# Kernel tuning notes

Measured on AMD Instinct MI355X. Metric: run time of the kernel, lower is better.

## Reference

```python
import jax, jax.numpy as jnp
import numpy as np

# Constants from __init__ (heston_info = [rho, theta, kappa, lambd], asset_info = [S0, V0, rate])
S0 = 100.0
V0 = 0.04
RATE = 0.025
THETA = 0.04
KAPPA = 1.5
LAMBD = 0.3
V_FLOOR = 0.01  # torch: V_old_abs = max(cat([V_new, zeros+0.01]), dim=1)

N_DIM = 3       # MLP input = [time, S, V]
N_LAYERS = 2
WIDTH = 50
MC = 65536
N_STEPS = 252
N_STRIKES = 13
N_MAT = 12


def setup_inputs() -> dict:
    key = jax.random.key(0)
    k = jax.random.split(key, 8)
    z = jax.random.normal(k[0], (MC, N_STEPS), dtype=jnp.float32)
    z1 = jax.random.normal(k[1], (MC, N_STEPS), dtype=jnp.float32)
    strikes_call = jnp.linspace(70.0, 100.0, N_STRIKES).astype(jnp.float32)
    strikes_put = jnp.linspace(100.0, 130.0, N_STRIKES).astype(jnp.float32)
    indices = jnp.arange(1, N_MAT + 1, dtype=jnp.int32) * (N_STEPS // N_MAT)  # monthly maturities
    timegrid = jnp.linspace(0.0, 1.0, N_STEPS + 1, dtype=jnp.float32)
    # 4 stacked MLPs: [drift, diffusion, driftV, diffusionV]; small init keeps the SDE stable
    s = 0.05
    W_in = s * jax.random.normal(k[2], (4, N_DIM, WIDTH), dtype=jnp.float32)
    b_in = jnp.zeros((4, WIDTH), jnp.float32)
    W_h = s * jax.random.normal(k[3], (4, N_LAYERS - 1, WIDTH, WIDTH), dtype=jnp.float32)
    b_h = jnp.zeros((4, N_LAYERS - 1, WIDTH), jnp.float32)
    W_out = 0.01 * jax.random.normal(k[4], (4, WIDTH, 1), dtype=jnp.float32)
    b_out = jnp.zeros((4, 1), jnp.float32)
    return dict(strikes_call=strikes_call, strikes_put=strikes_put, indices=indices,
                z=z, z1=z1, MC_samples=MC, timegrid=timegrid,
                W_in=W_in, b_in=b_in, W_h=W_h, b_h=b_h, W_out=W_out, b_out=b_out)


def _mlp4(x, W_in, b_in, W_h, b_h, W_out, b_out):
    # x: [mc, 3] -> [4, mc] (the 4 nets evaluated in one batched einsum)
    h = jax.nn.relu(jnp.einsum('mi,kio->kmo', x, W_in) + b_in[:, None, :])
    for l in range(W_h.shape[1]):
        h = jax.nn.relu(jnp.einsum('kmi,kio->kmo', h, W_h[:, l]) + b_h[:, l][:, None, :])
    return (jnp.einsum('kmi,kio->kmo', h, W_out) + b_out[:, None, :])[..., 0]


def _simulate(z, z1, timegrid, params, checkpoint=False):
    mc = z.shape[0]
    hstep = timegrid[1] - timegrid[0]
    sqh = jnp.sqrt(hstep)

    def step(carry, xs):
        S, V = carry
        t, zi, z1i = xs
        x = jnp.stack([jnp.broadcast_to(t, (mc,)), S, V], axis=1)  # inputNN = [time, S, V]
        drift, diff, driftV, diffV = _mlp4(x, *params)
        dW, dW1 = sqh * zi, sqh * z1i
        S_new = S + (S * RATE + drift) * hstep + (S * jnp.sqrt(V) + diff) * dW
        V_new = V + (KAPPA * (THETA - V) + driftV) * hstep + (LAMBD + diffV) * dW1
        V_new = jnp.maximum(V_new, V_FLOOR)
        return (S_new, V_new), S_new

    if checkpoint:
        step = jax.checkpoint(step)
    init = (jnp.full((mc,), S0, jnp.float32), jnp.full((mc,), V0, jnp.float32))
    _, S_path = jax.lax.scan(step, init, (timegrid[:-1], z.T, z1.T))
    return S_path  # [n_steps, mc]


def _prices(S_path, indices, timegrid, strikes_call, strikes_put):
    n_steps = timegrid.shape[0] - 1
    sel = S_path[indices - 1]  # [n_mat, mc]  (step i produces S after the i-th update)
    disc = jnp.exp(-RATE * indices.astype(jnp.float32) / n_steps)

    def avg(strikes):
        pay = jax.nn.relu(sel[:, :, None] - strikes[None, None, :]) * disc[:, None, None]
        return jnp.nanmean(pay, axis=1)  # [n_mat, n_strikes]

    # NOTE: the source uses max(S - K, 0) for BOTH the call and the put loops; kept faithful.
    return jnp.concatenate([avg(strikes_call), avg(strikes_put)], axis=0)


def reference(strikes_call, strikes_put, indices, z, z1, MC_samples, timegrid,
              W_in, b_in, W_h, b_h, W_out, b_out):
    params = (W_in, b_in, W_h, b_h, W_out, b_out)
    S_path = _simulate(z, z1, timegrid, params)
    return _prices(S_path, indices, timegrid, strikes_call, strikes_put)  # [2*n_mat, n_strikes]
```

## Files before the change

### kernel.cpp

```cpp
#include <hip/hip_runtime.h>
#include <hip/hip_bf16.h>
#include <math.h>


#define WIDTH   50
#define NSTRIDE 3200
#define O_WI    0
#define O_BI    160
#define O_WH    224
#define O_BH    3024
#define O_WO    3088
#define O_BO    3152
#define O_TG    12800
#define O_KC    13056
#define O_KP    13072
#define WSW_TOT 13088

typedef __attribute__((ext_vector_type(8)))  short        short8;
typedef __attribute__((ext_vector_type(4)))  short        short4v;
typedef __attribute__((ext_vector_type(16))) float        floatx16;
typedef __attribute__((ext_vector_type(4)))  unsigned int uint4v;
typedef __attribute__((ext_vector_type(2)))  unsigned int uint2v;
typedef __attribute__((ext_vector_type(2)))  float        float2v;
typedef __attribute__((ext_vector_type(4)))  float        float4v;

__device__ __forceinline__ float LDF(const void* p, size_t i, int f32)
{
    if (f32) return ((const float* __restrict__)p)[i];
    return __bfloat162float(((const __hip_bfloat16* __restrict__)p)[i]);
}

__device__ __forceinline__ unsigned short f2bf(float f)
{
    unsigned u = __builtin_bit_cast(unsigned, f);
    return (unsigned short)((u + 0x7FFFu + ((u >> 16) & 1u)) >> 16);
}
__device__ __forceinline__ unsigned pk2(float lo, float hi)
{
    return (unsigned)f2bf(lo) | ((unsigned)f2bf(hi) << 16);
}
__device__ __forceinline__ unsigned pk2t(float lo, float hi)
{
    return __builtin_amdgcn_perm(__builtin_bit_cast(unsigned, hi),
                                 __builtin_bit_cast(unsigned, lo),
                                 0x07060302u);
}

template<int R0>
__device__ __forceinline__ short8 mkB(floatx16 d)
{
    const float2v z2 = { 0.f, 0.f };
    float2v m0 = { d[R0 + 0], d[R0 + 1] };
    float2v m1 = { d[R0 + 2], d[R0 + 3] };
    float2v m2 = { d[R0 + 4], d[R0 + 5] };
    float2v m3 = { d[R0 + 6], d[R0 + 7] };
    m0 = __builtin_elementwise_max(m0, z2);
    m1 = __builtin_elementwise_max(m1, z2);
    m2 = __builtin_elementwise_max(m2, z2);
    m3 = __builtin_elementwise_max(m3, z2);
    const unsigned P0 = pk2t(m0.x, m0.y);
    const unsigned P1 = pk2t(m1.x, m1.y);
    const unsigned P2 = pk2t(m2.x, m2.y);
    const unsigned P3 = pk2t(m3.x, m3.y);
    const uint2v sA = __builtin_amdgcn_permlane32_swap(P0, P2, false, false);
    const uint2v sB = __builtin_amdgcn_permlane32_swap(P1, P3, false, false);
    const uint4v u = { sA.x, sB.x, sA.y, sB.y };
    return __builtin_bit_cast(short8, u);
}

__global__ void prep(const void* __restrict__ K13a, const void* __restrict__ K13b,
                     const void* __restrict__ p200a, const void* __restrict__ p200b,
                     const void* __restrict__ p200c,
                     const void* __restrict__ Win, const void* __restrict__ Wh,
                     const void* __restrict__ bout, const void* __restrict__ tg,
                     int* __restrict__ flags, float* __restrict__ wsw, int n_steps)
{
    __shared__ int sf[3];
    const int tid = threadIdx.x;
    if (tid == 0) {
        const unsigned int w0 = *(const unsigned int*)K13a;
        const int f32 = ((w0 & 0xFFFFu) == 0u) ? 1 : 0;
        sf[0] = f32;
        sf[1] = (LDF(K13a, 0, f32) > LDF(K13b, 0, f32)) ? 1 : 0;
        const void* P[3] = { p200a, p200b, p200c };
        float s0 = 0.f, s1 = 0.f, s2 = 0.f;
        for (int i = 0; i < 200; ++i) {
            s0 += fabsf(LDF(P[0], i, f32));
            s1 += fabsf(LDF(P[1], i, f32));
            s2 += fabsf(LDF(P[2], i, f32));
        }
        int wo = 0; float best = s0;
        if (s1 > best) { wo = 1; best = s1; }
        if (s2 > best) { wo = 2; }
        sf[2] = wo;
        flags[0] = f32; flags[1] = sf[1]; flags[2] = wo;
    }
    __syncthreads();
    const int f32 = sf[0], swap = sf[1], wo = sf[2];
    const void* Wout = (wo == 0) ? p200a : ((wo == 1) ? p200b : p200c);
    const void* bin  = (wo == 0) ? p200b : p200a;
    const void* bh   = (wo == 2) ? p200b : p200c;
    const void* Kc   = swap ? K13b : K13a;
    const void* Kp   = swap ? K13a : K13b;

    for (int i = tid; i < WSW_TOT; i += 256) wsw[i] = 0.f;
    __syncthreads();
    for (int i = tid; i < 600; i += 256) {
        int n = i / 150, rem = i % 150;
        wsw[n * NSTRIDE + O_WI + rem] = LDF(Win, i, f32);
    }
    for (int i = tid; i < 200; i += 256) {
        int n = i / 50, j = i % 50;
        wsw[n * NSTRIDE + O_BI + j] = LDF(bin, i, f32);
    }
    for (int i = tid; i < 10000; i += 256) {
        int n = i / 2500, rem = i % 2500, r = rem / 50, j = rem % 50;
        wsw[n * NSTRIDE + O_WH + r * 56 + j] = LDF(Wh, i, f32);
    }
    for (int i = tid; i < 200; i += 256) {
        int n = i / 50, j = i % 50;
        wsw[n * NSTRIDE + O_BH + j] = LDF(bh, i, f32);
    }
    for (int i = tid; i < 200; i += 256) {
        int n = i / 50, j = i % 50;
        wsw[n * NSTRIDE + O_WO + j] = LDF(Wout, i, f32);
    }
    if (tid < 4)  wsw[tid * NSTRIDE + O_BO] = LDF(bout, tid, f32);
    for (int i = tid; i <= n_steps; i += 256) wsw[O_TG + i] = LDF(tg, i, f32);
    if (tid < 13) { wsw[O_KC + tid] = LDF(Kc, tid, f32);
                    wsw[O_KP + tid] = LDF(Kp, tid, f32); }
}

__global__ __launch_bounds__(256, 3)
void sde_sim(const void* __restrict__ z,
             const void* __restrict__ z1,
             const int* __restrict__ indices,
             const int* __restrict__ flags,
             const float* __restrict__ wsw,
             float* __restrict__ acc_out,
             int n_steps, int n_mat)
{
    __shared__ float o_l[2][128];

    const int tid  = threadIdx.x;
    const int f32  = __builtin_amdgcn_readfirstlane(flags[0]);
    const int l    = tid & 63;
    const int q    = l & 31;
    const int h    = l >> 5;
    const int net  = __builtin_amdgcn_readfirstlane(tid >> 6);
    const float* __restrict__ Wb  = wsw + net * NSTRIDE;
    const float* __restrict__ TGp = wsw + O_TG;
    const float* __restrict__ KCp = wsw + O_KC;
    const float* __restrict__ KPp = wsw + O_KP;

    short8 A1[2];
    #pragma unroll
    for (int mt = 0; mt < 2; ++mt) {
        unsigned r01 = 0, r23 = 0;
        const int j = 32 * mt + q;
        if (h == 0 && j < WIDTH) {
            r01 = pk2(Wb[O_WI + j],       Wb[O_WI + 50 + j]);
            r23 = pk2(Wb[O_WI + 100 + j], Wb[O_BI + j]);
        }
        uint4v u = { r01, r23, 0u, 0u };
        A1[mt] = __builtin_bit_cast(short8, u);
    }
    short8 A2[2][4];
    #pragma unroll
    for (int mt = 0; mt < 2; ++mt) {
        const int j2 = 32 * mt + q;
        #pragma unroll
        for (int ks = 0; ks < 4; ++ks) {
            unsigned rr[4] = { 0u, 0u, 0u, 0u };
            if (j2 < WIDTH) {
                #pragma unroll
                for (int ii = 0; ii < 4; ++ii) {
                    const int k0 = 16 * ks + 8 * h + 2 * ii;
                    const int k1 = k0 + 1;
                    const float v0 = (k0 < WIDTH) ? Wb[O_WH + k0 * 56 + j2]
                                   : (k0 == 56 ? Wb[O_BH + j2] : 0.f);
                    const float v1 = (k1 < WIDTH) ? Wb[O_WH + k1 * 56 + j2]
                                   : (k1 == 56 ? Wb[O_BH + j2] : 0.f);
                    rr[ii] = pk2(v0, v1);
                }
            }
            uint4v u = { rr[0], rr[1], rr[2], rr[3] };
            A2[mt][ks] = __builtin_bit_cast(short8, u);
        }
    }
    float2v wv2a[8], wv2b[5];
    #pragma unroll
    for (int pr = 0; pr < 8; ++pr) {
        const int j2 = ((2 * pr) & 3) + 8 * ((2 * pr) >> 2) + 4 * h;
        wv2a[pr] = (float2v){ Wb[O_WO + j2], Wb[O_WO + j2 + 1] };
        if (pr < 5)
            wv2b[pr] = (float2v){ Wb[O_WO + 32 + j2], Wb[O_WO + 32 + j2 + 1] };
    }
    const float bo = Wb[O_BO];

    floatx16 Z;
    #pragma unroll
    for (int i = 0; i < 16; ++i) Z[i] = 0.f;

    const float hstep = TGp[1] - TGp[0];
    const float sqh   = sqrtf(hstep);
    float S = 100.0f, V = 0.04f;
    const int p = blockIdx.x * 32 + q;
    const size_t zbase = (size_t)p * (size_t)n_steps;

    int mi = 0;
    int mnext = (n_mat > 0) ? indices[0] : 0x7fffffff;

    for (int s0 = 0; s0 < n_steps; s0 += 4) {
        float zf[4], z1f[4];
        if (s0 + 4 <= n_steps) {
            if (f32) {
                const float4v a = *(const float4v*)((const float*)z  + zbase + s0);
                const float4v b = *(const float4v*)((const float*)z1 + zbase + s0);
                zf[0] = a.x; zf[1] = a.y; zf[2] = a.z; zf[3] = a.w;
                z1f[0] = b.x; z1f[1] = b.y; z1f[2] = b.z; z1f[3] = b.w;
            } else {
                const short4v a = *(const short4v*)((const __hip_bfloat16*)z  + zbase + s0);
                const short4v b = *(const short4v*)((const __hip_bfloat16*)z1 + zbase + s0);
                #pragma unroll
                for (int u = 0; u < 4; ++u) {
                    zf[u]  = __builtin_bit_cast(float, (unsigned)(unsigned short)a[u] << 16);
                    z1f[u] = __builtin_bit_cast(float, (unsigned)(unsigned short)b[u] << 16);
                }
            }
        } else {
            #pragma unroll
            for (int u = 0; u < 4; ++u) {
                zf[u]  = (s0 + u < n_steps) ? LDF(z,  zbase + s0 + u, f32) : 0.f;
                z1f[u] = (s0 + u < n_steps) ? LDF(z1, zbase + s0 + u, f32) : 0.f;
            }
        }
        const float4v t4 = *(const float4v*)(TGp + s0);

        #pragma unroll
        for (int u = 0; u < 4; ++u) {
            const int s = s0 + u;
            if (s < n_steps) {
                const float t = t4[u];

                uint4v bu = { pk2t(t, S), pk2t(V, 1.0f), 0u, 0u };
                const short8 B1 = __builtin_bit_cast(short8, bu);
                const floatx16 d1a =
                    __builtin_amdgcn_mfma_f32_32x32x16_bf16(A1[0], B1, Z, 0, 0, 0);

                floatx16 d2a, d2b;
                {   const short8 B = mkB<0>(d1a);
                    d2a = __builtin_amdgcn_mfma_f32_32x32x16_bf16(A2[0][0], B, Z, 0, 0, 0);
                    d2b = __builtin_amdgcn_mfma_f32_32x32x16_bf16(A2[1][0], B, Z, 0, 0, 0);
                }
                {   const short8 B = mkB<8>(d1a);
                    d2a = __builtin_amdgcn_mfma_f32_32x32x16_bf16(A2[0][1], B, d2a, 0, 0, 0);
                    d2b = __builtin_amdgcn_mfma_f32_32x32x16_bf16(A2[1][1], B, d2b, 0, 0, 0);
                }
                const floatx16 d1b =
                    __builtin_amdgcn_mfma_f32_32x32x16_bf16(A1[1], B1, Z, 0, 0, 0);
                {   const short8 B = mkB<0>(d1b);
                    d2a = __builtin_amdgcn_mfma_f32_32x32x16_bf16(A2[0][2], B, d2a, 0, 0, 0);
                    d2b = __builtin_amdgcn_mfma_f32_32x32x16_bf16(A2[1][2], B, d2b, 0, 0, 0);
                }
                {
                    const float2v z2 = { 0.f, 0.f };
                    float2v m0 = { d1b[8], d1b[9] };
                    m0 = __builtin_elementwise_max(m0, z2);
                    const unsigned P0 = pk2t(m0.x, m0.y);
                    const unsigned u0 = (h == 0) ? P0 : 0x00003F80u;
                    const uint4v ub = { u0, 0u, 0u, 0u };
                    const short8 B = __builtin_bit_cast(short8, ub);
                    d2a = __builtin_amdgcn_mfma_f32_32x32x16_bf16(A2[0][3], B, d2a, 0, 0, 0);
                    d2b = __builtin_amdgcn_mfma_f32_32x32x16_bf16(A2[1][3], B, d2b, 0, 0, 0);
                }

                const float2v z2 = { 0.f, 0.f };
                float2v acc2 = z2;
                #pragma unroll
                for (int pr = 0; pr < 8; ++pr) {
                    float2v v = { d2a[2 * pr], d2a[2 * pr + 1] };
                    v = __builtin_elementwise_max(v, z2);
                    acc2 = __builtin_elementwise_fma(v, wv2a[pr], acc2);
                }
                #pragma unroll
                for (int pr = 0; pr < 5; ++pr) {
                    float2v v = { d2b[2 * pr], d2b[2 * pr + 1] };
                    v = __builtin_elementwise_max(v, z2);
                    acc2 = __builtin_elementwise_fma(v, wv2b[pr], acc2);
                }
                float acc = acc2.x + acc2.y;
                acc += __shfl_xor(acc, 32, 64);
                const float o = acc + bo;

                float* ob = o_l[s & 1];
                ob[net * 32 + q] = o;
                __syncthreads();
                const float drift  = ob[q];
                const float diff   = ob[32 + q];
                const float driftV = ob[64 + q];
                const float diffV  = ob[96 + q];

                const float dW = sqh * zf[u], dW1 = sqh * z1f[u];
                const float Snew = S + (S * 0.025f + drift) * hstep
                                     + (S * sqrtf(V) + diff) * dW;
                const float Vnew = V + (1.5f * (0.04f - V) + driftV) * hstep
                                     + (0.3f + diffV) * dW1;
                S = Snew;
                V = fmaxf(Vnew, 0.01f);

                if (s + 1 == mnext) {
                    const int slot = mi;
                    ++mi;
                    mnext = (mi < n_mat) ? indices[mi] : 0x7fffffff;
                    #pragma unroll 1
                    for (int j = net; j < 13; j += 4) {
                        float pc = fmaxf(S - KCp[j], 0.f);
                        float pp = fmaxf(S - KPp[j], 0.f);
                        #pragma unroll
                        for (int off = 32; off > 0; off >>= 1) {
                            pc += __shfl_xor(pc, off, 64);
                            pp += __shfl_xor(pp, off, 64);
                        }
                        if (l == 0) {
                            atomicAdd(&acc_out[slot * 13 + j], pc);
                            atomicAdd(&acc_out[(n_mat + slot) * 13 + j], pp);
                        }
                    }
                }
            }
        }
    }
}

__global__ void finalize(const float* __restrict__ acc,
                         const int* __restrict__ indices,
                         const int* __restrict__ flags,
                         void* __restrict__ out,
                         int n_steps, int n_mat, float inv)
{
    const int t = threadIdx.x + blockIdx.x * blockDim.x;
    const int total = 2 * n_mat * 13;
    if (t < total) {
        const int row = t / 13;
        const int mat = row % n_mat;
        const float disc = expf(-0.025f * (float)indices[mat] / (float)n_steps);
        const float v = acc[t] * disc * inv;
        if (flags[0]) ((float*)out)[t] = v;
        else ((__hip_bfloat16*)out)[t] = __float2bfloat16(v);
    }
}

extern "C" void kernel_launch(void* const* d_in, const int* in_sizes, int n_in,
                              void* d_out, int out_size, void* d_ws, size_t ws_size,
                              hipStream_t stream)
{
    int i13a = 0, i13b = 1, iidx = 2, iz = 3, iz1 = 4, itg = 6, iwin = 7,
        iwh = 9, ibout = 12;
    int i200[3] = { 8, 10, 11 };
    int n13 = 0, nbig = 0, n200 = 0;
    int f13a = -1, f13b = -1, fidx = -1, fz = -1, fz1 = -1, ftg = -1,
        fwin = -1, fwh = -1, fbout = -1, f200[3] = { -1, -1, -1 };
    for (int i = 0; i < n_in; ++i) {
        const int s = in_sizes[i];
        if      (s == 13)      { if (n13 == 0) f13a = i; else if (n13 == 1) f13b = i; ++n13; }
        else if (s == 12)      fidx = i;
        else if (s == 253)     ftg = i;
        else if (s == 600)     fwin = i;
        else if (s == 10000)   fwh = i;
        else if (s == 4)       fbout = i;
        else if (s == 200)     { if (n200 < 3) f200[n200] = i; ++n200; }
        else if (s > 1000000)  { if (nbig == 0) fz = i; else if (nbig == 1) fz1 = i; ++nbig; }
    }
    if (f13a >= 0 && f13b >= 0 && fidx >= 0 && fz >= 0 && fz1 >= 0 && ftg >= 0 &&
        fwin >= 0 && fwh >= 0 && fbout >= 0 && f200[2] >= 0) {
        i13a = f13a; i13b = f13b; iidx = fidx; iz = fz; iz1 = fz1; itg = ftg;
        iwin = fwin; iwh = fwh; ibout = fbout;
        i200[0] = f200[0]; i200[1] = f200[1]; i200[2] = f200[2];
    }

    const void* K13a = d_in[i13a];
    const void* K13b = d_in[i13b];
    const int*  idx  = (const int*)d_in[iidx];
    const void* zz   = d_in[iz];
    const void* zz1  = d_in[iz1];
    const void* tg   = d_in[itg];
    const void* Win  = d_in[iwin];
    const void* Wh   = d_in[iwh];
    const void* bout = d_in[ibout];
    const void* p200a = d_in[i200[0]];
    const void* p200b = d_in[i200[1]];
    const void* p200c = d_in[i200[2]];

    const int n_steps = in_sizes[itg] - 1;
    const int n_mat   = in_sizes[iidx];
    const int mc      = in_sizes[iz] / n_steps;

    float* acc   = (float*)d_ws;
    int*   flags = (int*)((char*)d_ws + 2048);
    float* wsw   = (float*)((char*)d_ws + 4096);

    hipMemsetAsync(acc, 0, (size_t)(2 * n_mat * 13) * sizeof(float), stream);
    prep<<<1, 256, 0, stream>>>(K13a, K13b, p200a, p200b, p200c,
                                Win, Wh, bout, tg, flags, wsw, n_steps);

    const int blocks = mc / 32;
    sde_sim<<<blocks, 256, 0, stream>>>(zz, zz1, idx, flags, wsw, acc,
                                        n_steps, n_mat);

    finalize<<<1, 512, 0, stream>>>(acc, idx, flags, d_out,
                                    n_steps, n_mat, 0.5f / (float)mc);
}
```

Before: 1.479 ms.

## Process two path groups per block to interleave independent MFMA chains

Each block now simulates 64 paths as two independent 32-path groups whose MLP MFMA chains are interleaved, so one chain's latency can be hidden behind the other and the per-step block barrier is amortized over twice the work. The grid is halved, shared output staging is doubled, and launch bounds drop to 2 blocks per SM to allow more registers. The 4-step vectorized noise loads are replaced by per-step scalar loads, which adds load instructions and latency exposure. Lower occupancy may also reduce latency hiding across blocks.

```diff
diff --git a/kernel.cpp b/kernel.cpp
--- a/kernel.cpp
+++ b/kernel.cpp
@@ -17,12 +17,10 @@
 #define WSW_TOT 13088
 
 typedef __attribute__((ext_vector_type(8)))  short        short8;
-typedef __attribute__((ext_vector_type(4)))  short        short4v;
 typedef __attribute__((ext_vector_type(16))) float        floatx16;
 typedef __attribute__((ext_vector_type(4)))  unsigned int uint4v;
 typedef __attribute__((ext_vector_type(2)))  unsigned int uint2v;
 typedef __attribute__((ext_vector_type(2)))  float        float2v;
-typedef __attribute__((ext_vector_type(4)))  float        float4v;
 
 __device__ __forceinline__ float LDF(const void* p, size_t i, int f32)
 {
@@ -131,7 +129,7 @@
                     wsw[O_KP + tid] = LDF(Kp, tid, f32); }
 }
 
-__global__ __launch_bounds__(256, 3)
+__global__ __launch_bounds__(256, 2)
 void sde_sim(const void* __restrict__ z,
              const void* __restrict__ z1,
              const int* __restrict__ indices,
@@ -140,7 +138,7 @@
              float* __restrict__ acc_out,
              int n_steps, int n_mat)
 {
-    __shared__ float o_l[2][128];
+    __shared__ float o_l[2][256];
 
     const int tid  = threadIdx.x;
     const int f32  = __builtin_amdgcn_readfirstlane(flags[0]);
@@ -204,129 +202,159 @@
 
     const float hstep = TGp[1] - TGp[0];
     const float sqh   = sqrtf(hstep);
-    float S = 100.0f, V = 0.04f;
-    const int p = blockIdx.x * 32 + q;
-    const size_t zbase = (size_t)p * (size_t)n_steps;
+    float SA = 100.0f, VA = 0.04f;
+    float SB = 100.0f, VB = 0.04f;
+    const size_t zbaseA = (size_t)(blockIdx.x * 64 + q) * (size_t)n_steps;
+    const size_t zbaseB = zbaseA + (size_t)32 * (size_t)n_steps;
 
     int mi = 0;
     int mnext = (n_mat > 0) ? indices[0] : 0x7fffffff;
 
-    for (int s0 = 0; s0 < n_steps; s0 += 4) {
-        float zf[4], z1f[4];
-        if (s0 + 4 <= n_steps) {
-            if (f32) {
-                const float4v a = *(const float4v*)((const float*)z  + zbase + s0);
-                const float4v b = *(const float4v*)((const float*)z1 + zbase + s0);
-                zf[0] = a.x; zf[1] = a.y; zf[2] = a.z; zf[3] = a.w;
-                z1f[0] = b.x; z1f[1] = b.y; z1f[2] = b.z; z1f[3] = b.w;
-            } else {
-                const short4v a = *(const short4v*)((const __hip_bfloat16*)z  + zbase + s0);
-                const short4v b = *(const short4v*)((const __hip_bfloat16*)z1 + zbase + s0);
+    for (int s = 0; s < n_steps; ++s) {
+        const float zfA  = LDF(z,  zbaseA + s, f32);
+        const float z1fA = LDF(z1, zbaseA + s, f32);
+        const float zfB  = LDF(z,  zbaseB + s, f32);
+        const float z1fB = LDF(z1, zbaseB + s, f32);
+        const float t = TGp[s];
+
+        uint4v buA = { pk2t(t, SA), pk2t(VA, 1.0f), 0u, 0u };
+        uint4v buB = { pk2t(t, SB), pk2t(VB, 1.0f), 0u, 0u };
+        const short8 B1A = __builtin_bit_cast(short8, buA);
+        const short8 B1B = __builtin_bit_cast(short8, buB);
+        const floatx16 d1aA =
+            __builtin_amdgcn_mfma_f32_32x32x16_bf16(A1[0], B1A, Z, 0, 0, 0);
+        const floatx16 d1aB =
+            __builtin_amdgcn_mfma_f32_32x32x16_bf16(A1[0], B1B, Z, 0, 0, 0);
+
+        floatx16 d2aA, d2bA, d2aB, d2bB;
+        {   const short8 BA = mkB<0>(d1aA);
+            const short8 BB = mkB<0>(d1aB);
+            d2aA = __builtin_amdgcn_mfma_f32_32x32x16_bf16(A2[0][0], BA, Z, 0, 0, 0);
+            d2aB = __builtin_amdgcn_mfma_f32_32x32x16_bf16(A2[0][0], BB, Z, 0, 0, 0);
+            d2bA = __builtin_amdgcn_mfma_f32_32x32x16_bf16(A2[1][0], BA, Z, 0, 0, 0);
+            d2bB = __builtin_amdgcn_mfma_f32_32x32x16_bf16(A2[1][0], BB, Z, 0, 0, 0);
+        }
+        {   const short8 BA = mkB<8>(d1aA);
+            const short8 BB = mkB<8>(d1aB);
+            d2aA = __builtin_amdgcn_mfma_f32_32x32x16_bf16(A2[0][1], BA, d2aA, 0, 0, 0);
+            d2aB = __builtin_amdgcn_mfma_f32_32x32x16_bf16(A2[0][1], BB, d2aB, 0, 0, 0);
+            d2bA = __builtin_amdgcn_mfma_f32_32x32x16_bf16(A2[1][1], BA, d2bA, 0, 0, 0);
+            d2bB = __builtin_amdgcn_mfma_f32_32x32x16_bf16(A2[1][1], BB, d2bB, 0, 0, 0);
+        }
+        const floatx16 d1bA =
+            __builtin_amdgcn_mfma_f32_32x32x16_bf16(A1[1], B1A, Z, 0, 0, 0);
+        const floatx16 d1bB =
+            __builtin_amdgcn_mfma_f32_32x32x16_bf16(A1[1], B1B, Z, 0, 0, 0);
+        {   const short8 BA = mkB<0>(d1bA);
+            const short8 BB = mkB<0>(d1bB);
+            d2aA = __builtin_amdgcn_mfma_f32_32x32x16_bf16(A2[0][2], BA, d2aA, 0, 0, 0);
+            d2aB = __builtin_amdgcn_mfma_f32_32x32x16_bf16(A2[0][2], BB, d2aB, 0, 0, 0);
+            d2bA = __builtin_amdgcn_mfma_f32_32x32x16_bf16(A2[1][2], BA, d2bA, 0, 0, 0);
+            d2bB = __builtin_amdgcn_mfma_f32_32x32x16_bf16(A2[1][2], BB, d2bB, 0, 0, 0);
+        }
+        {
+            const float2v z2 = { 0.f, 0.f };
+            float2v mA = { d1bA[8], d1bA[9] };
+            float2v mB = { d1bB[8], d1bB[9] };
+            mA = __builtin_elementwise_max(mA, z2);
+            mB = __builtin_elementwise_max(mB, z2);
+            const unsigned uA0 = (h == 0) ? pk2t(mA.x, mA.y) : 0x00003F80u;
+            const unsigned uB0 = (h == 0) ? pk2t(mB.x, mB.y) : 0x00003F80u;
+            const uint4v ubA = { uA0, 0u, 0u, 0u };
+            const uint4v ubB = { uB0, 0u, 0u, 0u };
+            const short8 BA = __builtin_bit_cast(short8, ubA);
+            const short8 BB = __builtin_bit_cast(short8, ubB);
+            d2aA = __builtin_amdgcn_mfma_f32_32x32x16_bf16(A2[0][3], BA, d2aA, 0, 0, 0);
+            d2aB = __builtin_amdgcn_mfma_f32_32x32x16_bf16(A2[0][3], BB, d2aB, 0, 0, 0);
+            d2bA = __builtin_amdgcn_mfma_f32_32x32x16_bf16(A2[1][3], BA, d2bA, 0, 0, 0);
+            d2bB = __builtin_amdgcn_mfma_f32_32x32x16_bf16(A2[1][3], BB, d2bB, 0, 0, 0);
+        }
+
+        const float2v z2 = { 0.f, 0.f };
+        float2v accA2 = z2, accB2 = z2;
+        #pragma unroll
+        for (int pr = 0; pr < 8; ++pr) {
+            float2v vA = { d2aA[2 * pr], d2aA[2 * pr + 1] };
+            float2v vB = { d2aB[2 * pr], d2aB[2 * pr + 1] };
+            vA = __builtin_elementwise_max(vA, z2);
+            vB = __builtin_elementwise_max(vB, z2);
+            accA2 = __builtin_elementwise_fma(vA, wv2a[pr], accA2);
+            accB2 = __builtin_elementwise_fma(vB, wv2a[pr], accB2);
+        }
+        #pragma unroll
+        for (int pr = 0; pr < 5; ++pr) {
+            float2v vA = { d2bA[2 * pr], d2bA[2 * pr + 1] };
+            float2v vB = { d2bB[2 * pr], d2bB[2 * pr + 1] };
+            vA = __builtin_elementwise_max(vA, z2);
+            vB = __builtin_elementwise_max(vB, z2);
+            accA2 = __builtin_elementwise_fma(vA, wv2b[pr], accA2);
+            accB2 = __builtin_elementwise_fma(vB, wv2b[pr], accB2);
+        }
+        float accA = accA2.x + accA2.y;
+        float accB = accB2.x + accB2.y;
+        accA += __shfl_xor(accA, 32, 64);
+        accB += __shfl_xor(accB, 32, 64);
+        const float oA = accA + bo;
+        const float oB = accB + bo;
+
+        float* ob = o_l[s & 1];
+        ob[net * 32 + q]       = oA;
+        ob[128 + net * 32 + q] = oB;
+        __syncthreads();
+        const float driftA  = ob[q];
+        const float diffA   = ob[32 + q];
+        const float driftVA = ob[64 + q];
+        const float diffVA  = ob[96 + q];
+        const float driftB  = ob[128 + q];
+        const float diffB   = ob[160 + q];
+        const float driftVB = ob[192 + q];
+        const float diffVB  = ob[224 + q];
+
+        const float dWA = sqh * zfA, dW1A = sqh * z1fA;
+        const float SnewA = SA + (SA * 0.025f + driftA) * hstep
+                               + (SA * sqrtf(VA) + diffA) * dWA;
+        const float VnewA = VA + (1.5f * (0.04f - VA) + driftVA) * hstep
+                               + (0.3f + diffVA) * dW1A;
+        SA = SnewA;
+        VA = fmaxf(VnewA, 0.01f);
+        const float dWB = sqh * zfB, dW1B = sqh * z1fB;
+        const float SnewB = SB + (SB * 0.025f + driftB) * hstep
+                               + (SB * sqrtf(VB) + diffB) * dWB;
+        const float VnewB = VB + (1.5f * (0.04f - VB) + driftVB) * hstep
+                               + (0.3f + diffVB) * dW1B;
+        SB = SnewB;
+        VB = fmaxf(VnewB, 0.01f);
+
+        if (s + 1 == mnext) {
+            const int slot = mi;
+            ++mi;
+            mnext = (mi < n_mat) ? indices[mi] : 0x7fffffff;
+            #pragma unroll 1
+            for (int j = net; j < 13; j += 4) {
+                float pc = fmaxf(SA - KCp[j], 0.f);
+                float pp = fmaxf(SA - KPp[j], 0.f);
                 #pragma unroll
-                for (int u = 0; u < 4; ++u) {
-                    zf[u]  = __builtin_bit_cast(float, (unsigned)(unsigned short)a[u] << 16);
-                    z1f[u] = __builtin_bit_cast(float, (unsigned)(unsigned short)b[u] << 16);
+                for (int off = 32; off > 0; off >>= 1) {
+                    pc += __shfl_xor(pc, off, 64);
+                    pp += __shfl_xor(pp, off, 64);
+                }
+                if (l == 0) {
+                    atomicAdd(&acc_out[slot * 13 + j], pc);
+                    atomicAdd(&acc_out[(n_mat + slot) * 13 + j], pp);
                 }
             }
-        } else {
-            #pragma unroll
-            for (int u = 0; u < 4; ++u) {
-                zf[u]  = (s0 + u < n_steps) ? LDF(z,  zbase + s0 + u, f32) : 0.f;
-                z1f[u] = (s0 + u < n_steps) ? LDF(z1, zbase + s0 + u, f32) : 0.f;
-            }
-        }
-        const float4v t4 = *(const float4v*)(TGp + s0);
-
-        #pragma unroll
-        for (int u = 0; u < 4; ++u) {
-            const int s = s0 + u;
-            if (s < n_steps) {
-                const float t = t4[u];
-
-                uint4v bu = { pk2t(t, S), pk2t(V, 1.0f), 0u, 0u };
-                const short8 B1 = __builtin_bit_cast(short8, bu);
-                const floatx16 d1a =
-                    __builtin_amdgcn_mfma_f32_32x32x16_bf16(A1[0], B1, Z, 0, 0, 0);
-
-                floatx16 d2a, d2b;
-                {   const short8 B = mkB<0>(d1a);
-                    d2a = __builtin_amdgcn_mfma_f32_32x32x16_bf16(A2[0][0], B, Z, 0, 0, 0);
-                    d2b = __builtin_amdgcn_mfma_f32_32x32x16_bf16(A2[1][0], B, Z, 0, 0, 0);
+            #pragma unroll 1
+            for (int j = net; j < 13; j += 4) {
+                float pc = fmaxf(SB - KCp[j], 0.f);
+                float pp = fmaxf(SB - KPp[j], 0.f);
+                #pragma unroll
+                for (int off = 32; off > 0; off >>= 1) {
+                    pc += __shfl_xor(pc, off, 64);
+                    pp += __shfl_xor(pp, off, 64);
                 }
-                {   const short8 B = mkB<8>(d1a);
-                    d2a = __builtin_amdgcn_mfma_f32_32x32x16_bf16(A2[0][1], B, d2a, 0, 0, 0);
-                    d2b = __builtin_amdgcn_mfma_f32_32x32x16_bf16(A2[1][1], B, d2b, 0, 0, 0);
-                }
-                const floatx16 d1b =
-                    __builtin_amdgcn_mfma_f32_32x32x16_bf16(A1[1], B1, Z, 0, 0, 0);
-                {   const short8 B = mkB<0>(d1b);
-                    d2a = __builtin_amdgcn_mfma_f32_32x32x16_bf16(A2[0][2], B, d2a, 0, 0, 0);
-                    d2b = __builtin_amdgcn_mfma_f32_32x32x16_bf16(A2[1][2], B, d2b, 0, 0, 0);
-                }
-                {
-                    const float2v z2 = { 0.f, 0.f };
-                    float2v m0 = { d1b[8], d1b[9] };
-                    m0 = __builtin_elementwise_max(m0, z2);
-                    const unsigned P0 = pk2t(m0.x, m0.y);
-                    const unsigned u0 = (h == 0) ? P0 : 0x00003F80u;
-                    const uint4v ub = { u0, 0u, 0u, 0u };
-                    const short8 B = __builtin_bit_cast(short8, ub);
-                    d2a = __builtin_amdgcn_mfma_f32_32x32x16_bf16(A2[0][3], B, d2a, 0, 0, 0);
-                    d2b = __builtin_amdgcn_mfma_f32_32x32x16_bf16(A2[1][3], B, d2b, 0, 0, 0);
-                }
-
-                const float2v z2 = { 0.f, 0.f };
-                float2v acc2 = z2;
-                #pragma unroll
-                for (int pr = 0; pr < 8; ++pr) {
-                    float2v v = { d2a[2 * pr], d2a[2 * pr + 1] };
-                    v = __builtin_elementwise_max(v, z2);
-                    acc2 = __builtin_elementwise_fma(v, wv2a[pr], acc2);
-                }
-                #pragma unroll
-                for (int pr = 0; pr < 5; ++pr) {
-                    float2v v = { d2b[2 * pr], d2b[2 * pr + 1] };
-                    v = __builtin_elementwise_max(v, z2);
-                    acc2 = __builtin_elementwise_fma(v, wv2b[pr], acc2);
-                }
-                float acc = acc2.x + acc2.y;
-                acc += __shfl_xor(acc, 32, 64);
-                const float o = acc + bo;
-
-                float* ob = o_l[s & 1];
-                ob[net * 32 + q] = o;
-                __syncthreads();
-                const float drift  = ob[q];
-                const float diff   = ob[32 + q];
-                const float driftV = ob[64 + q];
-                const float diffV  = ob[96 + q];
-
-                const float dW = sqh * zf[u], dW1 = sqh * z1f[u];
-                const float Snew = S + (S * 0.025f + drift) * hstep
-                                     + (S * sqrtf(V) + diff) * dW;
-                const float Vnew = V + (1.5f * (0.04f - V) + driftV) * hstep
-                                     + (0.3f + diffV) * dW1;
-                S = Snew;
-                V = fmaxf(Vnew, 0.01f);
-
-                if (s + 1 == mnext) {
-                    const int slot = mi;
-                    ++mi;
-                    mnext = (mi < n_mat) ? indices[mi] : 0x7fffffff;
-                    #pragma unroll 1
-                    for (int j = net; j < 13; j += 4) {
-                        float pc = fmaxf(S - KCp[j], 0.f);
-                        float pp = fmaxf(S - KPp[j], 0.f);
-                        #pragma unroll
-                        for (int off = 32; off > 0; off >>= 1) {
-                            pc += __shfl_xor(pc, off, 64);
-                            pp += __shfl_xor(pp, off, 64);
-                        }
-                        if (l == 0) {
-                            atomicAdd(&acc_out[slot * 13 + j], pc);
-                            atomicAdd(&acc_out[(n_mat + slot) * 13 + j], pp);
-                        }
-                    }
+                if (l == 0) {
+                    atomicAdd(&acc_out[slot * 13 + j], pc);
+                    atomicAdd(&acc_out[(n_mat + slot) * 13 + j], pp);
                 }
             }
         }
@@ -404,7 +432,7 @@
     prep<<<1, 256, 0, stream>>>(K13a, K13b, p200a, p200b, p200c,
                                 Win, Wh, bout, tg, flags, wsw, n_steps);
 
-    const int blocks = mc / 32;
+    const int blocks = mc / 64;
     sde_sim<<<blocks, 256, 0, stream>>>(zz, zz1, idx, flags, wsw, acc,
                                         n_steps, n_mat);
 
```

Result: slower. 1.608 ms (+8.7%).
